# Optimization experiments

Measured on AMD Instinct MI355X. Metric: run time of the kernel, lower is better.

## Reference

```python
import jax, jax.numpy as jnp
import numpy as np

N_NODES = 100000
N_EDGES = 1250000
NFEAT = 64
NHID = 64


def setup_inputs() -> dict:
    key = jax.random.key(0)
    k1, k2, k3 = jax.random.split(key, 3)
    x = jax.random.normal(k1, (N_NODES, NFEAT), dtype=jnp.float32)
    edge_index = jax.random.randint(k2, (2, N_EDGES), 0, N_NODES, dtype=jnp.int64)
    # Glorot-style init for the GCNConv weight [out, in]
    scale = 1.0 / np.sqrt(NFEAT)
    weight = jax.random.normal(k3, (NHID, NFEAT), dtype=jnp.float32) * scale
    bias = jnp.zeros((NHID,), dtype=jnp.float32)
    return {"x": x, "edge_index": edge_index, "weight": weight, "bias": bias}


def reference(x, edge_index, weight, bias):
    """Single-layer GCNConv: out = D^-1/2 (A+I) D^-1/2 (x W^T) + b."""
    n = x.shape[0]
    # add self-loops
    loop = jnp.arange(n, dtype=edge_index.dtype)
    src = jnp.concatenate([edge_index[0], loop])  # [E+N]
    dst = jnp.concatenate([edge_index[1], loop])
    # linear transform first (cheaper: nfeat -> nhid)
    h = x @ weight.T  # [N, nhid]
    # symmetric normalization with unit edge weights
    ones = jnp.ones_like(dst, dtype=h.dtype)
    deg = jax.ops.segment_sum(ones, dst, num_segments=n)  # [N]
    dinv = jnp.where(deg > 0, jax.lax.rsqrt(jnp.maximum(deg, 1e-12)), 0.0)
    norm = dinv[src] * dinv[dst]  # [E+N]
    # gather -> scale -> scatter-add
    msg = h[src] * norm[:, None]  # [E+N, nhid]
    out = jax.ops.segment_sum(msg, dst, num_segments=n)  # [N, nhid]
    return out + bias
```

## Files before the change

kernel.cpp:

```cpp
#include <hip/hip_runtime.h>
#include <hip/hip_fp16.h>
#include <stdint.h>

#define NF 64

__global__ __launch_bounds__(256) void k_ell(const int* __restrict__ src,
                                             const int* __restrict__ dst,
                                             int* degc, int* ocnt, int* oflow, int ocap,
                                             int* ell, int e, int n) {
    int grp = blockIdx.x & 7;
    int chunk = (n + 7) >> 3;
    int lo = grp * chunk;
    int hi = min(lo + chunk, n);
    int nb = gridDim.x >> 3;
    int bi = blockIdx.x >> 3;
    for (int i = bi * 256 + threadIdx.x; i < e; i += nb * 256) {
        int d = dst[i];
        if (d < lo || d >= hi) continue;
        int s = src[i];
        int slot = atomicAdd(&degc[d], 1);
        if (slot < NF) {
            ell[(unsigned)d * NF + slot] = s;
        } else {
            int o = atomicAdd(ocnt, 1);
            if (o < ocap) { oflow[2 * o] = s; oflow[2 * o + 1] = d; }
        }
    }
}

__global__ __launch_bounds__(256) void k_scale(const float* __restrict__ x,
                                               const int* __restrict__ degc,
                                               __half* __restrict__ xh, int n) {
    int i = blockIdx.x * 256 + threadIdx.x;
    int total = (n + 1) * (NF / 4);
    if (i >= total) return;
    int row = i >> 4;
    uint2 u = {0u, 0u};
    if (row < n) {
        float dd = rsqrtf((float)(degc[row] + 1));
        float4 v = reinterpret_cast<const float4*>(x)[i];
        __half2 p0 = __floats2half2_rn(v.x * dd, v.y * dd);
        __half2 p1 = __floats2half2_rn(v.z * dd, v.w * dd);
        u.x = *reinterpret_cast<unsigned*>(&p0);
        u.y = *reinterpret_cast<unsigned*>(&p1);
    }
    reinterpret_cast<uint2*>(xh)[i] = u;
}


__global__ __launch_bounds__(256) void k_agg_gemm(const __half* __restrict__ xh,
                                                  const float* __restrict__ W,
                                                  const float* __restrict__ bias,
                                                  const int* __restrict__ degc,
                                                  float* out, int n) {
    __shared__ float wt[NF * NF];
    __shared__ float vsh[4][NF];
    int tid = threadIdx.x;
    for (int idx = tid; idx < NF * NF; idx += 256) {
        int k = idx >> 6, j = idx & 63;
        wt[idx] = W[j * NF + k];
    }
    int wv = tid >> 6;
    unsigned lane = tid & 63;
    float bj = bias[lane];
    __syncthreads();

    const int* outi = (const int*)out;
    int ngroups = (n + 3) >> 2, gs = gridDim.x;
    int g = blockIdx.x;
    int d = g * 4 + wv;
    int ev = 0, mc = 0;
    if (d < n) {
        ev = outi[(unsigned)d * NF + lane];
        mc = degc[d];
    }
    while (g < ngroups) {
        int gn = g + gs, dn = gn * 4 + wv;
        int evn = 0, mcn = 0;
        if (gn < ngroups && dn < n) {
            evn = outi[(unsigned)dn * NF + lane];
            mcn = degc[dn];
        }
        if (d < n) {
            float dd = rsqrtf((float)(mc + 1));
            int m = min(mc, NF);
            float a0 = __half2float(xh[(unsigned)d * NF + lane]);
            float a1 = 0.f, a2 = 0.f, a3 = 0.f, a4 = 0.f, a5 = 0.f, a6 = 0.f, a7 = 0.f;
            float a8 = 0.f, a9 = 0.f, a10 = 0.f, a11 = 0.f, a12 = 0.f, a13 = 0.f, a14 = 0.f, a15 = 0.f;
            for (int j = 0; j < m; j += 16) {
                int s0  = __shfl(ev, j + 0),  s1  = __shfl(ev, j + 1);
                int s2  = __shfl(ev, j + 2),  s3  = __shfl(ev, j + 3);
                int s4  = __shfl(ev, j + 4),  s5  = __shfl(ev, j + 5);
                int s6  = __shfl(ev, j + 6),  s7  = __shfl(ev, j + 7);
                int s8  = __shfl(ev, j + 8),  s9  = __shfl(ev, j + 9);
                int s10 = __shfl(ev, j + 10), s11 = __shfl(ev, j + 11);
                int s12 = __shfl(ev, j + 12), s13 = __shfl(ev, j + 13);
                int s14 = __shfl(ev, j + 14), s15 = __shfl(ev, j + 15);
                s0  = (j + 0  < m) ? s0  : n;  s1  = (j + 1  < m) ? s1  : n;
                s2  = (j + 2  < m) ? s2  : n;  s3  = (j + 3  < m) ? s3  : n;
                s4  = (j + 4  < m) ? s4  : n;  s5  = (j + 5  < m) ? s5  : n;
                s6  = (j + 6  < m) ? s6  : n;  s7  = (j + 7  < m) ? s7  : n;
                s8  = (j + 8  < m) ? s8  : n;  s9  = (j + 9  < m) ? s9  : n;
                s10 = (j + 10 < m) ? s10 : n;  s11 = (j + 11 < m) ? s11 : n;
                s12 = (j + 12 < m) ? s12 : n;  s13 = (j + 13 < m) ? s13 : n;
                s14 = (j + 14 < m) ? s14 : n;  s15 = (j + 15 < m) ? s15 : n;
                a0  += __half2float(xh[(unsigned)s0  * NF + lane]);
                a1  += __half2float(xh[(unsigned)s1  * NF + lane]);
                a2  += __half2float(xh[(unsigned)s2  * NF + lane]);
                a3  += __half2float(xh[(unsigned)s3  * NF + lane]);
                a4  += __half2float(xh[(unsigned)s4  * NF + lane]);
                a5  += __half2float(xh[(unsigned)s5  * NF + lane]);
                a6  += __half2float(xh[(unsigned)s6  * NF + lane]);
                a7  += __half2float(xh[(unsigned)s7  * NF + lane]);
                a8  += __half2float(xh[(unsigned)s8  * NF + lane]);
                a9  += __half2float(xh[(unsigned)s9  * NF + lane]);
                a10 += __half2float(xh[(unsigned)s10 * NF + lane]);
                a11 += __half2float(xh[(unsigned)s11 * NF + lane]);
                a12 += __half2float(xh[(unsigned)s12 * NF + lane]);
                a13 += __half2float(xh[(unsigned)s13 * NF + lane]);
                a14 += __half2float(xh[(unsigned)s14 * NF + lane]);
                a15 += __half2float(xh[(unsigned)s15 * NF + lane]);
            }
            float v = dd * ((((a0 + a1) + (a2 + a3)) + ((a4 + a5) + (a6 + a7)))
                          + (((a8 + a9) + (a10 + a11)) + ((a12 + a13) + (a14 + a15))));

            vsh[wv][lane] = v;
            float r = bj;
#pragma unroll
            for (int k0 = 0; k0 < NF; k0 += 4) {
                float4 bv = *reinterpret_cast<const float4*>(&vsh[wv][k0]);
                r = fmaf(bv.x, wt[(k0 + 0) * NF + lane], r);
                r = fmaf(bv.y, wt[(k0 + 1) * NF + lane], r);
                r = fmaf(bv.z, wt[(k0 + 2) * NF + lane], r);
                r = fmaf(bv.w, wt[(k0 + 3) * NF + lane], r);
            }
            out[(unsigned)d * NF + lane] = r;
        }
        g = gn; d = dn; ev = evn; mc = mcn;
    }
}

__global__ __launch_bounds__(64) void k_oflow(const float* __restrict__ x,
                                              const float* __restrict__ W,
                                              const int* __restrict__ degc,
                                              const int* __restrict__ ocnt,
                                              const int* __restrict__ oflow, int ocap,
                                              float* out) {
    int c = *ocnt; if (c > ocap) c = ocap;
    int lane = threadIdx.x;
    for (int o = blockIdx.x; o < c; o += gridDim.x) {
        int s = oflow[2 * o], d = oflow[2 * o + 1];
        float norm = rsqrtf((float)(degc[s] + 1)) * rsqrtf((float)(degc[d] + 1));
        float r = 0.f;
        for (int k = 0; k < NF; ++k)
            r = fmaf(x[(long)s * NF + k], W[lane * NF + k], r);
        atomicAdd(&out[(long)d * NF + lane], norm * r);
    }
}


extern "C" void kernel_launch(void* const* d_in, const int* in_sizes, int n_in,
                              void* d_out, int out_size, void* d_ws, size_t ws_size,
                              hipStream_t stream) {
    const float* x    = (const float*)d_in[0];
    const int*   ei   = (const int*)d_in[1];
    const float* W    = (const float*)d_in[2];
    const float* bias = (const float*)d_in[3];
    float*       out  = (float*)d_out;

    const int n = in_sizes[0] / NF;
    const int e = in_sizes[1] / 2;
    const int* src = ei;
    const int* dst = ei + e;

    int*    degc = (int*)d_ws;
    int*    ocnt = degc + n;
    uintptr_t p = ((uintptr_t)(ocnt + 1) + 255) & ~(uintptr_t)255;
    __half* xh   = (__half*)p;
    int*    oflow = (int*)(xh + (size_t)(n + 1) * NF);
    long    rest = (long)ws_size - ((char*)oflow - (char*)d_ws);
    int     ocap = rest > 0 ? (int)(rest / 8) : 0;

    dim3 blk(256);
    hipMemsetAsync(degc, 0, (size_t)(n + 1) * sizeof(int), stream);
    k_ell  <<<2048, blk, 0, stream>>>(src, dst, degc, ocnt, oflow, ocap, (int*)out, e, n);
    int total4 = (n + 1) * (NF / 4);
    k_scale<<<(total4 + 255) / 256, blk, 0, stream>>>(x, degc, xh, n);
    k_agg_gemm<<<2048, blk, 0, stream>>>(xh, W, bias, degc, out, n);
    k_oflow<<<64, 64, 0, stream>>>(x, W, degc, ocnt, oflow, ocap, out);
}
```

Measured before the change: 148.8 us.

## Gather neighbor rows with 8-byte vector loads across lane groups

The neighbor gather in the fused aggregation+GEMM kernel is restructured. Each wavefront now splits into four 16-lane groups, and each lane loads 4 halves (uint2) from a different neighbor row, instead of every lane loading a single half from each of 16 rows. Partial sums are reduced across the groups with xor shuffles, and one group writes the row to shared memory. This cuts the number of load instructions and shuffles per neighbor and widens the memory accesses, at the cost of a cross-lane reduction and a changed summation order.

```diff
diff --git a/kernel.cpp b/kernel.cpp
--- a/kernel.cpp
+++ b/kernel.cpp
@@ -62,6 +62,8 @@
     }
     int wv = tid >> 6;
     unsigned lane = tid & 63;
+    unsigned grp = lane >> 4;
+    unsigned fl  = lane & 15;
     float bj = bias[lane];
     __syncthreads();
 
@@ -84,47 +86,50 @@
         if (d < n) {
             float dd = rsqrtf((float)(mc + 1));
             int m = min(mc, NF);
-            float a0 = __half2float(xh[(unsigned)d * NF + lane]);
-            float a1 = 0.f, a2 = 0.f, a3 = 0.f, a4 = 0.f, a5 = 0.f, a6 = 0.f, a7 = 0.f;
-            float a8 = 0.f, a9 = 0.f, a10 = 0.f, a11 = 0.f, a12 = 0.f, a13 = 0.f, a14 = 0.f, a15 = 0.f;
+            float a0 = 0.f, a1 = 0.f, a2 = 0.f, a3 = 0.f;
+            float b0 = 0.f, b1 = 0.f, b2 = 0.f, b3 = 0.f;
+            float c0 = 0.f, c1 = 0.f, c2 = 0.f, c3 = 0.f;
+            float e0 = 0.f, e1 = 0.f, e2 = 0.f, e3 = 0.f;
             for (int j = 0; j < m; j += 16) {
-                int s0  = __shfl(ev, j + 0),  s1  = __shfl(ev, j + 1);
-                int s2  = __shfl(ev, j + 2),  s3  = __shfl(ev, j + 3);
-                int s4  = __shfl(ev, j + 4),  s5  = __shfl(ev, j + 5);
-                int s6  = __shfl(ev, j + 6),  s7  = __shfl(ev, j + 7);
-                int s8  = __shfl(ev, j + 8),  s9  = __shfl(ev, j + 9);
-                int s10 = __shfl(ev, j + 10), s11 = __shfl(ev, j + 11);
-                int s12 = __shfl(ev, j + 12), s13 = __shfl(ev, j + 13);
-                int s14 = __shfl(ev, j + 14), s15 = __shfl(ev, j + 15);
-                s0  = (j + 0  < m) ? s0  : n;  s1  = (j + 1  < m) ? s1  : n;
-                s2  = (j + 2  < m) ? s2  : n;  s3  = (j + 3  < m) ? s3  : n;
-                s4  = (j + 4  < m) ? s4  : n;  s5  = (j + 5  < m) ? s5  : n;
-                s6  = (j + 6  < m) ? s6  : n;  s7  = (j + 7  < m) ? s7  : n;
-                s8  = (j + 8  < m) ? s8  : n;  s9  = (j + 9  < m) ? s9  : n;
-                s10 = (j + 10 < m) ? s10 : n;  s11 = (j + 11 < m) ? s11 : n;
-                s12 = (j + 12 < m) ? s12 : n;  s13 = (j + 13 < m) ? s13 : n;
-                s14 = (j + 14 < m) ? s14 : n;  s15 = (j + 15 < m) ? s15 : n;
-                a0  += __half2float(xh[(unsigned)s0  * NF + lane]);
-                a1  += __half2float(xh[(unsigned)s1  * NF + lane]);
-                a2  += __half2float(xh[(unsigned)s2  * NF + lane]);
-                a3  += __half2float(xh[(unsigned)s3  * NF + lane]);
-                a4  += __half2float(xh[(unsigned)s4  * NF + lane]);
-                a5  += __half2float(xh[(unsigned)s5  * NF + lane]);
-                a6  += __half2float(xh[(unsigned)s6  * NF + lane]);
-                a7  += __half2float(xh[(unsigned)s7  * NF + lane]);
-                a8  += __half2float(xh[(unsigned)s8  * NF + lane]);
-                a9  += __half2float(xh[(unsigned)s9  * NF + lane]);
-                a10 += __half2float(xh[(unsigned)s10 * NF + lane]);
-                a11 += __half2float(xh[(unsigned)s11 * NF + lane]);
-                a12 += __half2float(xh[(unsigned)s12 * NF + lane]);
-                a13 += __half2float(xh[(unsigned)s13 * NF + lane]);
-                a14 += __half2float(xh[(unsigned)s14 * NF + lane]);
-                a15 += __half2float(xh[(unsigned)s15 * NF + lane]);
+                int i0 = j + (int)grp, i1 = j + 4 + (int)grp;
+                int i2 = j + 8 + (int)grp, i3 = j + 12 + (int)grp;
+                int s0 = __shfl(ev, i0); s0 = (i0 < m) ? s0 : n;
+                int s1 = __shfl(ev, i1); s1 = (i1 < m) ? s1 : n;
+                int s2 = __shfl(ev, i2); s2 = (i2 < m) ? s2 : n;
+                int s3 = __shfl(ev, i3); s3 = (i3 < m) ? s3 : n;
+                uint2 u0 = *reinterpret_cast<const uint2*>(xh + (unsigned)s0 * NF + fl * 4);
+                uint2 u1 = *reinterpret_cast<const uint2*>(xh + (unsigned)s1 * NF + fl * 4);
+                uint2 u2 = *reinterpret_cast<const uint2*>(xh + (unsigned)s2 * NF + fl * 4);
+                uint2 u3 = *reinterpret_cast<const uint2*>(xh + (unsigned)s3 * NF + fl * 4);
+                float2 f;
+                f = __half22float2(*reinterpret_cast<const __half2*>(&u0.x)); a0 += f.x; a1 += f.y;
+                f = __half22float2(*reinterpret_cast<const __half2*>(&u0.y)); a2 += f.x; a3 += f.y;
+                f = __half22float2(*reinterpret_cast<const __half2*>(&u1.x)); b0 += f.x; b1 += f.y;
+                f = __half22float2(*reinterpret_cast<const __half2*>(&u1.y)); b2 += f.x; b3 += f.y;
+                f = __half22float2(*reinterpret_cast<const __half2*>(&u2.x)); c0 += f.x; c1 += f.y;
+                f = __half22float2(*reinterpret_cast<const __half2*>(&u2.y)); c2 += f.x; c3 += f.y;
+                f = __half22float2(*reinterpret_cast<const __half2*>(&u3.x)); e0 += f.x; e1 += f.y;
+                f = __half22float2(*reinterpret_cast<const __half2*>(&u3.y)); e2 += f.x; e3 += f.y;
             }
-            float v = dd * ((((a0 + a1) + (a2 + a3)) + ((a4 + a5) + (a6 + a7)))
-                          + (((a8 + a9) + (a10 + a11)) + ((a12 + a13) + (a14 + a15))));
-
-            vsh[wv][lane] = v;
+            uint2 us = *reinterpret_cast<const uint2*>(xh + (unsigned)d * NF + fl * 4);
+            float2 fs0 = __half22float2(*reinterpret_cast<const __half2*>(&us.x));
+            float2 fs1 = __half22float2(*reinterpret_cast<const __half2*>(&us.y));
+            a0 = (a0 + b0) + (c0 + e0);
+            a1 = (a1 + b1) + (c1 + e1);
+            a2 = (a2 + b2) + (c2 + e2);
+            a3 = (a3 + b3) + (c3 + e3);
+            a0 += __shfl_xor(a0, 16); a1 += __shfl_xor(a1, 16);
+            a2 += __shfl_xor(a2, 16); a3 += __shfl_xor(a3, 16);
+            a0 += __shfl_xor(a0, 32); a1 += __shfl_xor(a1, 32);
+            a2 += __shfl_xor(a2, 32); a3 += __shfl_xor(a3, 32);
+            if (grp == 0) {
+                float4 v4;
+                v4.x = dd * (a0 + fs0.x);
+                v4.y = dd * (a1 + fs0.y);
+                v4.z = dd * (a2 + fs1.x);
+                v4.w = dd * (a3 + fs1.y);
+                *reinterpret_cast<float4*>(&vsh[wv][fl * 4]) = v4;
+            }
             float r = bj;
 #pragma unroll
             for (int k0 = 0; k0 < NF; k0 += 4) {
```

Measured after the change: 146.0 us. About the same (-1.9%).
